# Performance work log

Hardware: AMD Instinct MI355X
Metric: run time of the kernel (lower is better)

The kernel has to match this reference:

```python
import jax, jax.numpy as jnp
import numpy as np

HIDDEN = 512
BATCH = 64
SEQ = 1024


def setup_inputs() -> dict:
    key = jax.random.key(0)
    ks = jax.random.split(key, 16)
    H = HIDDEN
    s = 0.05
    inp = {
        'x': jax.random.normal(ks[0], (BATCH, SEQ), dtype=jnp.float32),
        # layer 1: input size 1
        'W_ih1': jax.random.normal(ks[1], (4 * H, 1), dtype=jnp.float32) * s,
        'W_hh1': jax.random.normal(ks[2], (4 * H, H), dtype=jnp.float32) * s,
        'b_ih1': jax.random.normal(ks[3], (4 * H,), dtype=jnp.float32) * s,
        'b_hh1': jax.random.normal(ks[4], (4 * H,), dtype=jnp.float32) * s,
        # layer 2
        'W_ih2': jax.random.normal(ks[5], (4 * H, H), dtype=jnp.float32) * s,
        'W_hh2': jax.random.normal(ks[6], (4 * H, H), dtype=jnp.float32) * s,
        'b_ih2': jax.random.normal(ks[7], (4 * H,), dtype=jnp.float32) * s,
        'b_hh2': jax.random.normal(ks[8], (4 * H,), dtype=jnp.float32) * s,
        # layer 3
        'W_ih3': jax.random.normal(ks[9], (4 * H, H), dtype=jnp.float32) * s,
        'W_hh3': jax.random.normal(ks[10], (4 * H, H), dtype=jnp.float32) * s,
        'b_ih3': jax.random.normal(ks[11], (4 * H,), dtype=jnp.float32) * s,
        'b_hh3': jax.random.normal(ks[12], (4 * H,), dtype=jnp.float32) * s,
        # output projection
        'W_lin': jax.random.normal(ks[13], (1, H), dtype=jnp.float32) * s,
        'b_lin': jax.random.normal(ks[14], (1,), dtype=jnp.float32) * s,
    }
    return inp


def _lstm_cell(x, h, c, W_ih, W_hh, b_ih, b_hh):
    # PyTorch LSTMCell: gates ordered [i, f, g, o]
    gates = x @ W_ih.T + b_ih + h @ W_hh.T + b_hh  # [B, 4H]
    i, f, g, o = jnp.split(gates, 4, axis=-1)
    i = jax.nn.sigmoid(i)
    f = jax.nn.sigmoid(f)
    g = jnp.tanh(g)
    o = jax.nn.sigmoid(o)
    c_new = f * c + i * g
    h_new = o * jnp.tanh(c_new)
    return h_new, c_new


def reference(x, W_ih1, W_hh1, b_ih1, b_hh1,
              W_ih2, W_hh2, b_ih2, b_hh2,
              W_ih3, W_hh3, b_ih3, b_hh3,
              W_lin, b_lin):
    B = x.shape[0]
    H = W_hh1.shape[1]
    z = jnp.zeros((B, H), dtype=x.dtype)
    init = (z, z, z, z, z, z)  # h1,c1,h2,c2,h3,c3

    def step(carry, x_t):
        h1, c1, h2, c2, h3, c3 = carry
        h1, c1 = _lstm_cell(x_t, h1, c1, W_ih1, W_hh1, b_ih1, b_hh1)
        h2, c2 = _lstm_cell(h1, h2, c2, W_ih2, W_hh2, b_ih2, b_hh2)
        h3, c3 = _lstm_cell(h2, h3, c3, W_ih3, W_hh3, b_ih3, b_hh3)
        out = h3 @ W_lin.T + b_lin  # [B, 1]
        return (h1, c1, h2, c2, h3, c3), out

    xs = x.T[:, :, None]  # [T, B, 1]
    _, outs = jax.lax.scan(step, init, xs)  # outs: [T, B, 1]
    return outs[:, :, 0].T  # [B, T]
```

## Files before the change

### kernel.cpp

```cpp
#include <hip/hip_runtime.h>
#include <cstdint>
#include <cstddef>


typedef __attribute__((ext_vector_type(8))) short bf16x8;
typedef __attribute__((ext_vector_type(4))) float f32x4;
typedef __attribute__((ext_vector_type(2))) unsigned long long u64x2;

#define TT    1024
#define RINGD 8
#define NBL   64
#define NGRID (3*NBL + 1)
#define SENT  0xFFFFFFFFu

#define OFF_W1   0ULL
#define OFF_W2   (OFF_W1 + 2048ULL*512*2)
#define OFF_W3   (OFF_W2 + 2048ULL*1024*2)
#define OFF_BIAS (OFF_W3 + 2048ULL*1024*2)
#define OFF_FLAG (OFF_BIAS + 3ULL*2048*4)
#define OFF_RING (OFF_FLAG + 4096ULL)
#define NEED_BIG (OFF_RING + 3ULL*TT*64*512*2)

__device__ __forceinline__ unsigned short f2bf(float f) {
  unsigned int u = __float_as_uint(f);
  unsigned int r = (u + 0x7fffu + ((u >> 16) & 1u)) >> 16;
  return (unsigned short)r;
}
__device__ __forceinline__ float bf2f(unsigned short h) {
  return __uint_as_float(((unsigned int)h) << 16);
}
__device__ __forceinline__ float sigmf_(float z) {
  return 1.f / (1.f + __expf(-z));
}
__device__ __forceinline__ float tanhf_(float z) {
  float t = __expf(-2.f * fabsf(z));
  float r = (1.f - t) / (1.f + t);
  return (z < 0.f) ? -r : r;
}
__device__ __forceinline__ int badq(unsigned long long v) {
  return (int)(((unsigned int)v == SENT) | ((unsigned int)(v >> 32) == SENT));
}

__global__ void prep_kernel(const float* __restrict__ wih1, const float* __restrict__ whh1,
                            const float* __restrict__ bih1, const float* __restrict__ bhh1,
                            const float* __restrict__ wih2, const float* __restrict__ whh2,
                            const float* __restrict__ bih2, const float* __restrict__ bhh2,
                            const float* __restrict__ wih3, const float* __restrict__ whh3,
                            const float* __restrict__ bih3, const float* __restrict__ bhh3,
                            unsigned char* ws, int big)
{
  unsigned short* w1 = (unsigned short*)(ws + OFF_W1);
  unsigned short* w2 = (unsigned short*)(ws + OFF_W2);
  unsigned short* w3 = (unsigned short*)(ws + OFF_W3);
  float* bias = (float*)(ws + OFF_BIAS);
  int*   flags = (int*)(ws + OFF_FLAG);
  int idx = blockIdx.x * 256 + threadIdx.x;
  int j = idx >> 10, k = idx & 1023;
  if (j < 2048) {
    float v2 = (k < 512) ? wih2[j*512 + k] : whh2[j*512 + (k - 512)];
    float v3 = (k < 512) ? wih3[j*512 + k] : whh3[j*512 + (k - 512)];
    w2[j*1024 + k] = f2bf(v2);
    w3[j*1024 + k] = f2bf(v3);
    if (k < 512) w1[j*512 + k] = f2bf(whh1[j*512 + k]);
  }
  if (idx < 2048) {
    bias[idx]        = bih1[idx] + bhh1[idx];
    bias[2048 + idx] = bih2[idx] + bhh2[idx];
    bias[4096 + idx] = bih3[idx] + bhh3[idx];
  }
  if (idx < 256) flags[idx] = 0;
  if (big) {
    uint4* r4 = (uint4*)(ws + OFF_RING);
    uint4 s; s.x = SENT; s.y = SENT; s.z = SENT; s.w = SENT;
    for (size_t i = idx; i < 12582912ULL; i += 2097152ULL) r4[i] = s;
  }
}

template<int KSTEPS>
__device__ __forceinline__ void compute_tiles(const bf16x8 (&warr)[32], const char* smemc,
                                              int wv, int ln15, int kgrp,
                                              f32x4 (&acc)[2][4])
{
  const int k0w = wv * (KSTEPS * 32);
  const int sw  = (ln15 & 7) << 4;
  #pragma unroll
  for (int s = 0; s < KSTEPS; ++s) {
    const int koff = k0w + s*32 + kgrp*8;
    const int r    = koff >> 9;
    const int kin  = koff & 511;
    const char* ab = smemc + r*32768;
    bf16x8 a0 = *(const bf16x8*)(ab + ((ln15*1024        + kin*2) ^ sw));
    bf16x8 a1 = *(const bf16x8*)(ab + (((ln15 + 16)*1024 + kin*2) ^ sw));
    #pragma unroll
    for (int gt = 0; gt < 4; ++gt) {
      acc[0][gt] = __builtin_amdgcn_mfma_f32_16x16x32_bf16(a0, warr[gt*KSTEPS + s], acc[0][gt], 0, 0, 0);
      acc[1][gt] = __builtin_amdgcn_mfma_f32_16x16x32_bf16(a1, warr[gt*KSTEPS + s], acc[1][gt], 0, 0, 0);
    }
  }
}

__global__ __launch_bounds__(256, 1) void rnn_kernel(
    unsigned char* ws, const float* __restrict__ x,
    const float* __restrict__ wih1, const float* __restrict__ wlin,
    const float* __restrict__ blin, float* __restrict__ out, int big)
{
  __shared__ __align__(128) char smem[98304];
  const int tid  = threadIdx.x;
  const int lane = tid & 63;
  const int wv   = tid >> 6;
  const int SLOTS = big ? TT : RINGD;
  int* flags = (int*)(ws + OFF_FLAG);
  unsigned int* ringw = (unsigned int*)(ws + OFF_RING);
  const unsigned long long* ringq = (const unsigned long long*)(ws + OFF_RING);

  if (blockIdx.x == NGRID - 1) {
    float* wl = (float*)smem;
    float* op = (float*)(smem + 4096);
    if (tid < 128) ((f32x4*)wl)[tid] = ((const f32x4*)wlin)[tid];
    float blv = blin[0];
    __syncthreads();
    const int ob = tid >> 2, okq = tid & 3;
    const int* fup = flags + 2*64 + lane;
    for (int t = 0; t < TT; ++t) {
      if (!big && wv == 0) {
        for (;;) {
          int v = __hip_atomic_load(fup, __ATOMIC_RELAXED, __HIP_MEMORY_SCOPE_AGENT);
          if (__all(v >= t + 1)) break;
          __builtin_amdgcn_s_sleep(2);
        }
      }
      asm volatile("" ::: "memory");
      __syncthreads();
      const int slot = big ? t : (t & 7);
      size_t ebase = ((size_t)(2*SLOTS + slot) * 64 + ob) * 512 + (size_t)okq * 128;
      const unsigned long long* hp = ringq + (ebase >> 2);
      const float* wlp = wl + okq * 128;
      unsigned long long qv[32];
      if (big) {
        #pragma unroll
        for (int i = 0; i < 32; ++i) qv[i] = hp[i];
        for (;;) {
          int bad = 0;
          #pragma unroll
          for (int i = 0; i < 32; ++i) bad |= badq(qv[i]);
          if (!bad) break;
          __builtin_amdgcn_s_sleep(2);
          #pragma unroll
          for (int i = 0; i < 32; ++i)
            qv[i] = __hip_atomic_load(hp + i, __ATOMIC_RELAXED, __HIP_MEMORY_SCOPE_AGENT);
        }
      } else {
        #pragma unroll
        for (int i = 0; i < 32; ++i)
          qv[i] = __hip_atomic_load(hp + i, __ATOMIC_RELAXED, __HIP_MEMORY_SCOPE_AGENT);
      }
      float acc = 0.f;
      #pragma unroll
      for (int i = 0; i < 32; ++i) {
        acc += bf2f((unsigned short)(qv[i]      )) * wlp[i*4 + 0];
        acc += bf2f((unsigned short)(qv[i] >> 16)) * wlp[i*4 + 1];
        acc += bf2f((unsigned short)(qv[i] >> 32)) * wlp[i*4 + 2];
        acc += bf2f((unsigned short)(qv[i] >> 48)) * wlp[i*4 + 3];
      }
      op[ob*4 + okq] = acc;
      __syncthreads();
      if (tid < 64)
        out[(size_t)tid * TT + t] = op[tid*4] + op[tid*4+1] + op[tid*4+2] + op[tid*4+3] + blv;
      if (!big && tid == 0)
        __hip_atomic_store(flags + 3*64, t + 1, __ATOMIC_RELEASE, __HIP_MEMORY_SCOPE_AGENT);
      __syncthreads();
    }
    return;
  }

  const int g  = blockIdx.x >> 6;
  const int q  = blockIdx.x & 63;
  const int bh = q & 1;
  const int nbase = (q >> 1) << 4;
  const unsigned short* Wg =
      (const unsigned short*)(ws + (g == 0 ? OFF_W1 : (g == 1 ? OFF_W2 : OFF_W3)));
  const float* biasg = (const float*)(ws + OFF_BIAS) + g * 2048;

  const int ln15 = lane & 15;
  const int kgrp = lane >> 4;

  bf16x8 warr[32];
  if (g == 0) {
    #pragma unroll
    for (int gt = 0; gt < 4; ++gt)
      #pragma unroll
      for (int s = 0; s < 4; ++s)
        warr[gt*4 + s] = *(const bf16x8*)(Wg + (size_t)(gt*512 + nbase + ln15)*512
                                             + wv*128 + s*32 + kgrp*8);
  } else {
    #pragma unroll
    for (int gt = 0; gt < 4; ++gt)
      #pragma unroll
      for (int s = 0; s < 8; ++s)
        warr[gt*8 + s] = *(const bf16x8*)(Wg + (size_t)(gt*512 + nbase + ln15)*1024
                                             + wv*256 + s*32 + kgrp*8);
  }

  const int eb  = tid >> 3;
  const int n0  = (tid & 7) << 1;
  const int bge = bh * 32 + eb;
  float bsv[4][2], wxv[4][2];
  #pragma unroll
  for (int gt = 0; gt < 4; ++gt) {
    #pragma unroll
    for (int cc = 0; cc < 2; ++cc) {
      int jj = gt*512 + nbase + n0 + cc;
      bsv[gt][cc] = biasg[jj];
      wxv[gt][cc] = (g == 0) ? wih1[jj] : 0.f;
    }
  }
  float cst0 = 0.f, cst1 = 0.f;

  const int l31 = lane & 31;
  int* myflag = flags + g*64 + q;
  const int* fup  = flags + (g > 0 ? (g - 1)*64 : 0) + 2*l31 + bh;
  const int* fsib = flags + g*64 + 2*l31 + bh;
  const int* fdn  = (g < 2) ? (flags + (g + 1)*64 + 2*l31 + bh) : (flags + 3*64);

  const int sbi = tid >> 3, skc = tid & 7;
  const int swz = (sbi & 7) << 4;
  char* dstR0 = smem + sbi*1024;
  char* dstR1 = smem + 32768 + sbi*1024;
  char* dstP  = (g == 0) ? dstR0 : dstR1;
  float* part = (float*)(smem + 65536);

  auto stage_big = [&](int gg, int tick, char* dst) {
    size_t ebase = ((size_t)(gg*TT + tick) * 64 + bh*32 + sbi) * 512;
    const unsigned long long* src = ringq + (ebase >> 2);
    unsigned long long v[16];
    #pragma unroll
    for (int i = 0; i < 8; ++i) {
      v[2*i]   = src[(i*8 + skc)*2];
      v[2*i+1] = src[(i*8 + skc)*2 + 1];
    }
    for (;;) {
      int bad = 0;
      #pragma unroll
      for (int i = 0; i < 16; ++i) bad |= badq(v[i]);
      if (!bad) break;
      __builtin_amdgcn_s_sleep(2);
      #pragma unroll
      for (int i = 0; i < 8; ++i) {
        v[2*i]   = __hip_atomic_load(src + (i*8 + skc)*2,     __ATOMIC_RELAXED, __HIP_MEMORY_SCOPE_AGENT);
        v[2*i+1] = __hip_atomic_load(src + (i*8 + skc)*2 + 1, __ATOMIC_RELAXED, __HIP_MEMORY_SCOPE_AGENT);
      }
    }
    #pragma unroll
    for (int i = 0; i < 8; ++i) {
      u64x2 w; w[0] = v[2*i]; w[1] = v[2*i+1];
      *(u64x2*)(dst + (((i*8 + skc) * 16) ^ swz)) = w;
    }
  };
  auto stage_small = [&](int gg, int slot, char* dst) {
    size_t ebase = ((size_t)(gg*RINGD + slot) * 64 + bh*32 + sbi) * 512;
    const unsigned long long* src = ringq + (ebase >> 2);
    unsigned long long v[16];
    #pragma unroll
    for (int i = 0; i < 16; ++i)
      v[i] = __hip_atomic_load(src + (i*8 + skc), __ATOMIC_RELAXED, __HIP_MEMORY_SCOPE_AGENT);
    #pragma unroll
    for (int i = 0; i < 16; ++i)
      *(unsigned long long*)(dst + (((i*8 + skc) * 8) ^ swz)) = v[i];
  };
  auto zero_row = [&](char* dst) {
    #pragma unroll
    for (int i = 0; i < 16; ++i)
      *(unsigned long long*)(dst + (((i*8 + skc) * 8) ^ swz)) = 0ULL;
  };

  if (g > 0) {
    if (big) {
      stage_big(g - 1, 0, dstR0);
    } else {
      if (wv == 0) {
        for (;;) {
          int v = __hip_atomic_load(fup, __ATOMIC_RELAXED, __HIP_MEMORY_SCOPE_AGENT);
          if (__all(v >= 1)) break;
          __builtin_amdgcn_s_sleep(2);
        }
      }
      asm volatile("" ::: "memory");
      __syncthreads();
      stage_small(g - 1, 0, dstR0);
    }
  }

  for (int t = 0; t < TT; ++t) {
    const int slot = big ? t : (t & 7);
    if (!big) {
      if (wv == 0) {
        for (;;) {
          int ok = 1;
          if (t >= 1) {
            int v = __hip_atomic_load(fsib, __ATOMIC_RELAXED, __HIP_MEMORY_SCOPE_AGENT);
            ok &= (v >= t);
          }
          if (t >= RINGD) {
            int v = __hip_atomic_load(fdn, __ATOMIC_RELAXED, __HIP_MEMORY_SCOPE_AGENT);
            ok &= (v >= t - RINGD + 1);
          }
          if (__all(ok)) break;
          __builtin_amdgcn_s_sleep(2);
        }
      }
      asm volatile("" ::: "memory");
      __syncthreads();
    }
    if (t == 0)   zero_row(dstP);
    else if (big) stage_big(g, t - 1, dstP);
    else          stage_small(g, (t - 1) & 7, dstP);
    __syncthreads();

    f32x4 acc[2][4];
    #pragma unroll
    for (int a = 0; a < 2; ++a) {
      #pragma unroll
      for (int b = 0; b < 4; ++b) { f32x4 z = {0.f, 0.f, 0.f, 0.f}; acc[a][b] = z; }
    }
    if (g == 0) compute_tiles<4>(warr, smem, wv, ln15, kgrp, acc);
    else        compute_tiles<8>(warr, smem, wv, ln15, kgrp, acc);

    #pragma unroll
    for (int bt = 0; bt < 2; ++bt) {
      #pragma unroll
      for (int gt = 0; gt < 4; ++gt) {
        #pragma unroll
        for (int rr = 0; rr < 4; ++rr) {
          int brow = bt*16 + kgrp*4 + rr;
          int jj   = gt*16 + ln15;
          part[(wv*32 + brow)*64 + (jj ^ ((brow & 3) << 4))] = acc[bt][gt][rr];
        }
      }
    }
    __syncthreads();

    float Gv[4][2];
    #pragma unroll
    for (int gt = 0; gt < 4; ++gt) {
      #pragma unroll
      for (int cc = 0; cc < 2; ++cc) {
        int jx = (gt*16 + n0 + cc) ^ ((eb & 3) << 4);
        Gv[gt][cc] = part[(0*32 + eb)*64 + jx] + part[(1*32 + eb)*64 + jx]
                   + part[(2*32 + eb)*64 + jx] + part[(3*32 + eb)*64 + jx]
                   + bsv[gt][cc];
      }
    }
    if (g == 0) {
      float xv = x[(size_t)bge * TT + t];
      #pragma unroll
      for (int gt = 0; gt < 4; ++gt) {
        Gv[gt][0] += xv * wxv[gt][0];
        Gv[gt][1] += xv * wxv[gt][1];
      }
    }
    float i0 = sigmf_(Gv[0][0]), f0 = sigmf_(Gv[1][0]), gA = tanhf_(Gv[2][0]), o0 = sigmf_(Gv[3][0]);
    float i1 = sigmf_(Gv[0][1]), f1 = sigmf_(Gv[1][1]), gB = tanhf_(Gv[2][1]), o1 = sigmf_(Gv[3][1]);
    cst0 = f0 * cst0 + i0 * gA;
    cst1 = f1 * cst1 + i1 * gB;
    float h0 = o0 * tanhf_(cst0);
    float h1 = o1 * tanhf_(cst1);
    unsigned int packed = (unsigned int)f2bf(h0) | ((unsigned int)f2bf(h1) << 16);
    size_t eidx = ((size_t)(g*SLOTS + slot) * 64 + bge) * 512 + nbase + n0;
    __hip_atomic_store(ringw + (eidx >> 1), packed, __ATOMIC_RELAXED, __HIP_MEMORY_SCOPE_AGENT);

    if (!big) {
      __syncthreads();
      if (tid == 0)
        __hip_atomic_store(myflag, t + 1, __ATOMIC_RELEASE, __HIP_MEMORY_SCOPE_AGENT);
    }

    if (g > 0 && t + 1 < TT) {
      if (big) {
        stage_big(g - 1, t + 1, dstR0);
      } else {
        if (wv == 0) {
          for (;;) {
            int v = __hip_atomic_load(fup, __ATOMIC_RELAXED, __HIP_MEMORY_SCOPE_AGENT);
            if (__all(v >= t + 2)) break;
            __builtin_amdgcn_s_sleep(2);
          }
        }
        asm volatile("" ::: "memory");
        __syncthreads();
        stage_small(g - 1, (t + 1) & 7, dstR0);
      }
    }
    if (!big) __syncthreads();
  }
}

extern "C" void kernel_launch(void* const* d_in, const int* in_sizes, int n_in,
                              void* d_out, int out_size, void* d_ws, size_t ws_size,
                              hipStream_t stream)
{
  const float* x    = (const float*)d_in[0];
  const float* wih1 = (const float*)d_in[1];
  const float* whh1 = (const float*)d_in[2];
  const float* bih1 = (const float*)d_in[3];
  const float* bhh1 = (const float*)d_in[4];
  const float* wih2 = (const float*)d_in[5];
  const float* whh2 = (const float*)d_in[6];
  const float* bih2 = (const float*)d_in[7];
  const float* bhh2 = (const float*)d_in[8];
  const float* wih3 = (const float*)d_in[9];
  const float* whh3 = (const float*)d_in[10];
  const float* bih3 = (const float*)d_in[11];
  const float* bhh3 = (const float*)d_in[12];
  const float* wlin = (const float*)d_in[13];
  const float* blin = (const float*)d_in[14];
  unsigned char* ws = (unsigned char*)d_ws;
  float* out = (float*)d_out;

  int big = (ws_size >= NEED_BIG) ? 1 : 0;

  hipLaunchKernelGGL(prep_kernel, dim3(8192), dim3(256), 0, stream,
                     wih1, whh1, bih1, bhh1, wih2, whh2, bih2, bhh2,
                     wih3, whh3, bih3, bhh3, ws, big);

  static_assert(NGRID == 193, "grid");
  void* kws = (void*)ws;  void* kx = (void*)x;  void* kw1 = (void*)wih1;
  void* kwl = (void*)wlin; void* kbl = (void*)blin; void* ko = (void*)out;
  void* args[] = { &kws, &kx, &kw1, &kwl, &kbl, &ko, &big };
  hipError_t lerr = hipLaunchCooperativeKernel((void*)rnn_kernel, dim3(NGRID),
                                               dim3(256), args, 0, stream);
  if (lerr != hipSuccess) {
    hipLaunchKernelGGL(rnn_kernel, dim3(NGRID), dim3(256), 0, stream,
                       ws, x, wih1, wlin, blin, out, big);
  }
}
```

Measured before the change: 3.852 ms.

## Load MFMA A-fragments directly from ring buffer, skipping LDS staging in big mode

In the big-workspace path, each wave now loads its bf16 input fragments straight from the global ring buffer into registers and polls for sentinel values per fragment, instead of staging whole rows into shared memory first. This drops the LDS copy and the barriers around it. The partial-sum scratch area is double-buffered across timesteps so one barrier per step can be removed. The cost is less coalesced global loads and a per-wave spin on possibly partly written data, which could raise latency on the serial critical path.

```diff
diff --git a/kernel.cpp b/kernel.cpp
--- a/kernel.cpp
+++ b/kernel.cpp
@@ -5,7 +5,7 @@
 
 typedef __attribute__((ext_vector_type(8))) short bf16x8;
 typedef __attribute__((ext_vector_type(4))) float f32x4;
-typedef __attribute__((ext_vector_type(2))) unsigned long long u64x2;
+typedef __attribute__((ext_vector_type(4))) unsigned int u32x4;
 
 #define TT    1024
 #define RINGD 8
@@ -39,6 +39,21 @@
 }
 __device__ __forceinline__ int badq(unsigned long long v) {
   return (int)(((unsigned int)v == SENT) | ((unsigned int)(v >> 32) == SENT));
+}
+__device__ __forceinline__ int bad4(u32x4 v) {
+  return (int)((v[0] == SENT) | (v[1] == SENT) | (v[2] == SENT) | (v[3] == SENT));
+}
+__device__ __forceinline__ bf16x8 asbf(u32x4 v) {
+  union { u32x4 u; bf16x8 b; } c; c.u = v; return c.b;
+}
+__device__ __forceinline__ u32x4 ld16a(const unsigned short* p) {
+  const unsigned long long* q = (const unsigned long long*)p;
+  unsigned long long lo = __hip_atomic_load(q,     __ATOMIC_RELAXED, __HIP_MEMORY_SCOPE_AGENT);
+  unsigned long long hi = __hip_atomic_load(q + 1, __ATOMIC_RELAXED, __HIP_MEMORY_SCOPE_AGENT);
+  u32x4 r;
+  r[0] = (unsigned int)lo; r[1] = (unsigned int)(lo >> 32);
+  r[2] = (unsigned int)hi; r[3] = (unsigned int)(hi >> 32);
+  return r;
 }
 
 __global__ void prep_kernel(const float* __restrict__ wih1, const float* __restrict__ whh1,
@@ -99,6 +114,54 @@
   }
 }
 
+template<int KS>
+__device__ __forceinline__ void direct_tiles(const bf16x8 (&warr)[32],
+                                             const unsigned short* rowIn,
+                                             const unsigned short* rowPrev,
+                                             int wv, int ln15, int kgrp,
+                                             f32x4 (&acc)[2][4])
+{
+  u32x4 f0[KS], f1[KS];
+  const int k0w = wv * (KS * 32);
+  #pragma unroll
+  for (int s = 0; s < KS; ++s) {
+    const int koff = k0w + s*32 + kgrp*8;
+    const unsigned short* src = (KS == 4) ? rowPrev : ((koff < 512) ? rowIn : rowPrev);
+    const int kin = (KS == 4) ? koff : (koff & 511);
+    if (src) {
+      f0[s] = *(const u32x4*)(src + (size_t)ln15*512 + kin);
+      f1[s] = *(const u32x4*)(src + (size_t)(ln15 + 16)*512 + kin);
+    } else {
+      u32x4 z = {0u, 0u, 0u, 0u}; f0[s] = z; f1[s] = z;
+    }
+  }
+  for (;;) {
+    int bad = 0;
+    #pragma unroll
+    for (int s = 0; s < KS; ++s) bad |= bad4(f0[s]) | bad4(f1[s]);
+    if (!__any(bad)) break;
+    __builtin_amdgcn_s_sleep(2);
+    #pragma unroll
+    for (int s = 0; s < KS; ++s) {
+      const int koff = k0w + s*32 + kgrp*8;
+      const unsigned short* src = (KS == 4) ? rowPrev : ((koff < 512) ? rowIn : rowPrev);
+      const int kin = (KS == 4) ? koff : (koff & 511);
+      if (src) {
+        f0[s] = ld16a(src + (size_t)ln15*512 + kin);
+        f1[s] = ld16a(src + (size_t)(ln15 + 16)*512 + kin);
+      }
+    }
+  }
+  #pragma unroll
+  for (int s = 0; s < KS; ++s) {
+    #pragma unroll
+    for (int gt = 0; gt < 4; ++gt) {
+      acc[0][gt] = __builtin_amdgcn_mfma_f32_16x16x32_bf16(asbf(f0[s]), warr[gt*KS + s], acc[0][gt], 0, 0, 0);
+      acc[1][gt] = __builtin_amdgcn_mfma_f32_16x16x32_bf16(asbf(f1[s]), warr[gt*KS + s], acc[1][gt], 0, 0, 0);
+    }
+  }
+}
+
 __global__ __launch_bounds__(256, 1) void rnn_kernel(
     unsigned char* ws, const float* __restrict__ x,
     const float* __restrict__ wih1, const float* __restrict__ wlin,
@@ -111,6 +174,7 @@
   const int SLOTS = big ? TT : RINGD;
   int* flags = (int*)(ws + OFF_FLAG);
   unsigned int* ringw = (unsigned int*)(ws + OFF_RING);
+  unsigned short* ring16 = (unsigned short*)(ws + OFF_RING);
   const unsigned long long* ringq = (const unsigned long long*)(ws + OFF_RING);
 
   if (blockIdx.x == NGRID - 1) {
@@ -224,107 +288,8 @@
 
   const int sbi = tid >> 3, skc = tid & 7;
   const int swz = (sbi & 7) << 4;
-  char* dstR0 = smem + sbi*1024;
-  char* dstR1 = smem + 32768 + sbi*1024;
-  char* dstP  = (g == 0) ? dstR0 : dstR1;
-  float* part = (float*)(smem + 65536);
-
-  auto stage_big = [&](int gg, int tick, char* dst) {
-    size_t ebase = ((size_t)(gg*TT + tick) * 64 + bh*32 + sbi) * 512;
-    const unsigned long long* src = ringq + (ebase >> 2);
-    unsigned long long v[16];
-    #pragma unroll
-    for (int i = 0; i < 8; ++i) {
-      v[2*i]   = src[(i*8 + skc)*2];
-      v[2*i+1] = src[(i*8 + skc)*2 + 1];
-    }
-    for (;;) {
-      int bad = 0;
-      #pragma unroll
-      for (int i = 0; i < 16; ++i) bad |= badq(v[i]);
-      if (!bad) break;
-      __builtin_amdgcn_s_sleep(2);
-      #pragma unroll
-      for (int i = 0; i < 8; ++i) {
-        v[2*i]   = __hip_atomic_load(src + (i*8 + skc)*2,     __ATOMIC_RELAXED, __HIP_MEMORY_SCOPE_AGENT);
-        v[2*i+1] = __hip_atomic_load(src + (i*8 + skc)*2 + 1, __ATOMIC_RELAXED, __HIP_MEMORY_SCOPE_AGENT);
-      }
-    }
-    #pragma unroll
-    for (int i = 0; i < 8; ++i) {
-      u64x2 w; w[0] = v[2*i]; w[1] = v[2*i+1];
-      *(u64x2*)(dst + (((i*8 + skc) * 16) ^ swz)) = w;
-    }
-  };
-  auto stage_small = [&](int gg, int slot, char* dst) {
-    size_t ebase = ((size_t)(gg*RINGD + slot) * 64 + bh*32 + sbi) * 512;
-    const unsigned long long* src = ringq + (ebase >> 2);
-    unsigned long long v[16];
-    #pragma unroll
-    for (int i = 0; i < 16; ++i)
-      v[i] = __hip_atomic_load(src + (i*8 + skc), __ATOMIC_RELAXED, __HIP_MEMORY_SCOPE_AGENT);
-    #pragma unroll
-    for (int i = 0; i < 16; ++i)
-      *(unsigned long long*)(dst + (((i*8 + skc) * 8) ^ swz)) = v[i];
-  };
-  auto zero_row = [&](char* dst) {
-    #pragma unroll
-    for (int i = 0; i < 16; ++i)
-      *(unsigned long long*)(dst + (((i*8 + skc) * 8) ^ swz)) = 0ULL;
-  };
-
-  if (g > 0) {
-    if (big) {
-      stage_big(g - 1, 0, dstR0);
-    } else {
-      if (wv == 0) {
-        for (;;) {
-          int v = __hip_atomic_load(fup, __ATOMIC_RELAXED, __HIP_MEMORY_SCOPE_AGENT);
-          if (__all(v >= 1)) break;
-          __builtin_amdgcn_s_sleep(2);
-        }
-      }
-      asm volatile("" ::: "memory");
-      __syncthreads();
-      stage_small(g - 1, 0, dstR0);
-    }
-  }
-
-  for (int t = 0; t < TT; ++t) {
-    const int slot = big ? t : (t & 7);
-    if (!big) {
-      if (wv == 0) {
-        for (;;) {
-          int ok = 1;
-          if (t >= 1) {
-            int v = __hip_atomic_load(fsib, __ATOMIC_RELAXED, __HIP_MEMORY_SCOPE_AGENT);
-            ok &= (v >= t);
-          }
-          if (t >= RINGD) {
-            int v = __hip_atomic_load(fdn, __ATOMIC_RELAXED, __HIP_MEMORY_SCOPE_AGENT);
-            ok &= (v >= t - RINGD + 1);
-          }
-          if (__all(ok)) break;
-          __builtin_amdgcn_s_sleep(2);
-        }
-      }
-      asm volatile("" ::: "memory");
-      __syncthreads();
-    }
-    if (t == 0)   zero_row(dstP);
-    else if (big) stage_big(g, t - 1, dstP);
-    else          stage_small(g, (t - 1) & 7, dstP);
-    __syncthreads();
-
-    f32x4 acc[2][4];
-    #pragma unroll
-    for (int a = 0; a < 2; ++a) {
-      #pragma unroll
-      for (int b = 0; b < 4; ++b) { f32x4 z = {0.f, 0.f, 0.f, 0.f}; acc[a][b] = z; }
-    }
-    if (g == 0) compute_tiles<4>(warr, smem, wv, ln15, kgrp, acc);
-    else        compute_tiles<8>(warr, smem, wv, ln15, kgrp, acc);
-
+
+  auto cell_epilogue = [&](f32x4 (&acc)[2][4], float* part, int t, int slot) {
     #pragma unroll
     for (int bt = 0; bt < 2; ++bt) {
       #pragma unroll
@@ -338,7 +303,6 @@
       }
     }
     __syncthreads();
-
     float Gv[4][2];
     #pragma unroll
     for (int gt = 0; gt < 4; ++gt) {
@@ -367,30 +331,115 @@
     unsigned int packed = (unsigned int)f2bf(h0) | ((unsigned int)f2bf(h1) << 16);
     size_t eidx = ((size_t)(g*SLOTS + slot) * 64 + bge) * 512 + nbase + n0;
     __hip_atomic_store(ringw + (eidx >> 1), packed, __ATOMIC_RELAXED, __HIP_MEMORY_SCOPE_AGENT);
-
-    if (!big) {
+  };
+
+  if (big) {
+    for (int t = 0; t < TT; ++t) {
+      const unsigned short* rowIn = (g > 0)
+        ? ring16 + (((size_t)((g-1)*TT + t) * 64 + bh*32) * 512) : (const unsigned short*)0;
+      const unsigned short* rowPrev = (t > 0)
+        ? ring16 + (((size_t)(g*TT + (t-1)) * 64 + bh*32) * 512) : (const unsigned short*)0;
+
+      f32x4 acc[2][4];
+      #pragma unroll
+      for (int a = 0; a < 2; ++a) {
+        #pragma unroll
+        for (int b = 0; b < 4; ++b) { f32x4 z = {0.f, 0.f, 0.f, 0.f}; acc[a][b] = z; }
+      }
+      if (g == 0) direct_tiles<4>(warr, (const unsigned short*)0, rowPrev, wv, ln15, kgrp, acc);
+      else        direct_tiles<8>(warr, rowIn, rowPrev, wv, ln15, kgrp, acc);
+
+      float* part = (float*)(smem + ((t & 1) ? 0 : 65536));
+      cell_epilogue(acc, part, t, t);
+    }
+    return;
+  }
+
+  auto stage_small = [&](int gg, int slot, char* dst) {
+    size_t ebase = ((size_t)(gg*RINGD + slot) * 64 + bh*32 + sbi) * 512;
+    const unsigned long long* src = ringq + (ebase >> 2);
+    unsigned long long v[16];
+    #pragma unroll
+    for (int i = 0; i < 16; ++i)
+      v[i] = __hip_atomic_load(src + (i*8 + skc), __ATOMIC_RELAXED, __HIP_MEMORY_SCOPE_AGENT);
+    #pragma unroll
+    for (int i = 0; i < 16; ++i)
+      *(unsigned long long*)(dst + (((i*8 + skc) * 8) ^ swz)) = v[i];
+  };
+  auto zero_row = [&](char* dst) {
+    #pragma unroll
+    for (int i = 0; i < 16; ++i)
+      *(unsigned long long*)(dst + (((i*8 + skc) * 8) ^ swz)) = 0ULL;
+  };
+  char* dstR0 = smem + sbi*1024;
+  char* dstR1 = smem + 32768 + sbi*1024;
+  char* dstP  = (g == 0) ? dstR0 : dstR1;
+  float* partS = (float*)(smem + 65536);
+
+  if (g > 0) {
+    if (wv == 0) {
+      for (;;) {
+        int v = __hip_atomic_load(fup, __ATOMIC_RELAXED, __HIP_MEMORY_SCOPE_AGENT);
+        if (__all(v >= 1)) break;
+        __builtin_amdgcn_s_sleep(2);
+      }
+    }
+    asm volatile("" ::: "memory");
+    __syncthreads();
+    stage_small(g - 1, 0, dstR0);
+  }
+
+  for (int t = 0; t < TT; ++t) {
+    const int slot = t & 7;
+    if (wv == 0) {
+      for (;;) {
+        int ok = 1;
+        if (t >= 1) {
+          int v = __hip_atomic_load(fsib, __ATOMIC_RELAXED, __HIP_MEMORY_SCOPE_AGENT);
+          ok &= (v >= t);
+        }
+        if (t >= RINGD) {
+          int v = __hip_atomic_load(fdn, __ATOMIC_RELAXED, __HIP_MEMORY_SCOPE_AGENT);
+          ok &= (v >= t - RINGD + 1);
+        }
+        if (__all(ok)) break;
+        __builtin_amdgcn_s_sleep(2);
+      }
+    }
+    asm volatile("" ::: "memory");
+    __syncthreads();
+    if (t == 0) zero_row(dstP);
+    else        stage_small(g, (t - 1) & 7, dstP);
+    __syncthreads();
+
+    f32x4 acc[2][4];
+    #pragma unroll
+    for (int a = 0; a < 2; ++a) {
+      #pragma unroll
+      for (int b = 0; b < 4; ++b) { f32x4 z = {0.f, 0.f, 0.f, 0.f}; acc[a][b] = z; }
+    }
+    if (g == 0) compute_tiles<4>(warr, smem, wv, ln15, kgrp, acc);
+    else        compute_tiles<8>(warr, smem, wv, ln15, kgrp, acc);
+    __syncthreads();
+
+    cell_epilogue(acc, partS, t, slot);
+    __syncthreads();
+    if (tid == 0)
+      __hip_atomic_store(myflag, t + 1, __ATOMIC_RELEASE, __HIP_MEMORY_SCOPE_AGENT);
+
+    if (g > 0 && t + 1 < TT) {
+      if (wv == 0) {
+        for (;;) {
+          int v = __hip_atomic_load(fup, __ATOMIC_RELAXED, __HIP_MEMORY_SCOPE_AGENT);
+          if (__all(v >= t + 2)) break;
+          __builtin_amdgcn_s_sleep(2);
+        }
+      }
+      asm volatile("" ::: "memory");
       __syncthreads();
-      if (tid == 0)
-        __hip_atomic_store(myflag, t + 1, __ATOMIC_RELEASE, __HIP_MEMORY_SCOPE_AGENT);
-    }
-
-    if (g > 0 && t + 1 < TT) {
-      if (big) {
-        stage_big(g - 1, t + 1, dstR0);
-      } else {
-        if (wv == 0) {
-          for (;;) {
-            int v = __hip_atomic_load(fup, __ATOMIC_RELAXED, __HIP_MEMORY_SCOPE_AGENT);
-            if (__all(v >= t + 2)) break;
-            __builtin_amdgcn_s_sleep(2);
-          }
-        }
-        asm volatile("" ::: "memory");
-        __syncthreads();
-        stage_small(g - 1, (t + 1) & 7, dstR0);
-      }
-    }
-    if (!big) __syncthreads();
+      stage_small(g - 1, (t + 1) & 7, dstR0);
+    }
+    __syncthreads();
   }
 }
 
```

Result: slower. 7.115 ms (+84.7%).
